# Optimization experiments

Measured on AMD Instinct MI355X. Metric: run time of the kernel, lower is better.

Reference implementation:

```python
import jax, jax.numpy as jnp
import numpy as np

N = 100000
E = 3200000
IN_DIM = 128
HD = 64
HEADS = 4
NEG_SLOPE = 0.2


def setup_inputs() -> dict:
    key = jax.random.key(0)
    ks = jax.random.split(key, 12)
    s = lambda fan_in: 1.0 / np.sqrt(fan_in)
    x = jax.random.normal(ks[0], (N, IN_DIM), dtype=jnp.float32)
    edge_index = jax.random.randint(ks[1], (2, E), 0, N, dtype=jnp.int64)
    W1 = jax.random.normal(ks[2], (IN_DIM, HEADS * HD), dtype=jnp.float32) * s(IN_DIM)
    a_src1 = jax.random.normal(ks[3], (HEADS, HD), dtype=jnp.float32) * s(HD)
    a_dst1 = jax.random.normal(ks[4], (HEADS, HD), dtype=jnp.float32) * s(HD)
    b1 = jnp.zeros((HEADS * HD,), dtype=jnp.float32)
    W2 = jax.random.normal(ks[5], (HEADS * HD, HD), dtype=jnp.float32) * s(HEADS * HD)
    a_src2 = jax.random.normal(ks[6], (1, HD), dtype=jnp.float32) * s(HD)
    a_dst2 = jax.random.normal(ks[7], (1, HD), dtype=jnp.float32) * s(HD)
    b2 = jnp.zeros((HD,), dtype=jnp.float32)
    lin_w = jax.random.normal(ks[8], (HD, 2), dtype=jnp.float32) * s(HD)
    lin_b = jnp.zeros((2,), dtype=jnp.float32)
    return {"x": x, "edge_index": edge_index, "W1": W1, "a_src1": a_src1,
            "a_dst1": a_dst1, "b1": b1, "W2": W2, "a_src2": a_src2,
            "a_dst2": a_dst2, "b2": b2, "lin_w": lin_w, "lin_b": lin_b}


def gat_conv(x, src, dst, W, a_src, a_dst, bias, heads, out_dim, concat):
    n = x.shape[0]
    h = (x @ W).reshape(n, heads, out_dim)                 # [N,H,D]
    alpha_s = jnp.einsum('nhd,hd->nh', h, a_src)           # [N,H]
    alpha_d = jnp.einsum('nhd,hd->nh', h, a_dst)           # [N,H]
    e = alpha_s[src] + alpha_d[dst]                        # [Etot,H]
    e = jnp.where(e > 0, e, NEG_SLOPE * e)                 # leaky relu
    m = jax.ops.segment_max(e, dst, num_segments=n)        # scatter-softmax (stable)
    m = jnp.where(jnp.isfinite(m), m, 0.0)
    e = jnp.exp(e - m[dst])
    denom = jax.ops.segment_sum(e, dst, num_segments=n)
    alpha = e / denom[dst]                                 # [Etot,H]
    out = jax.ops.segment_sum(h[src] * alpha[:, :, None], dst, num_segments=n)  # [N,H,D]
    out = out.reshape(n, heads * out_dim) if concat else out.mean(axis=1)
    return out + bias


def reference(x, edge_index, W1, a_src1, a_dst1, b1, W2, a_src2, a_dst2, b2, lin_w, lin_b):
    n = x.shape[0]
    loops = jnp.arange(n, dtype=edge_index.dtype)
    src = jnp.concatenate([edge_index[0], loops])          # add self-loops (PyG default)
    dst = jnp.concatenate([edge_index[1], loops])
    h = gat_conv(x, src, dst, W1, a_src1, a_dst1, b1, HEADS, HD, True)
    h = jax.nn.elu(h)
    h = gat_conv(h, src, dst, W2, a_src2, a_dst2, b2, 1, HD, True)
    h = jax.nn.elu(h)
    return h @ lin_w + lin_b                               # [N,2]
```

## Files before the change

### kernel.cpp

```cpp
#include <hip/hip_runtime.h>
#include <hip/hip_fp16.h>
#include <math.h>

#define NN 100000
#define EE 3200000
#define ETOT (EE + NN)
#define NEG_SLOPE 0.2f
#define DMAX 96
#define CHUNK 4096
#define NB0 ((ETOT + CHUNK - 1) / CHUNK)
#define RB 391
#define CAP 16384
#define PREPB 391

typedef _Float16 half8 __attribute__((ext_vector_type(8)));
typedef _Float16 half4v __attribute__((ext_vector_type(4)));
typedef float floatx4 __attribute__((ext_vector_type(4)));

__device__ __forceinline__ float wsum64(float v) {
#pragma unroll
  for (int o = 32; o; o >>= 1) v += __shfl_xor(v, o);
  return v;
}
__device__ __forceinline__ float lrelu(float v) { return v > 0.f ? v : NEG_SLOPE * v; }
__device__ __forceinline__ float elu1(float v) { return v > 0.f ? v : expm1f(v); }

__global__ void k_init(int* __restrict__ ccur) {
  ccur[threadIdx.x] = threadIdx.x * CAP;
}

__global__ __launch_bounds__(256) void k_pass1(const int* __restrict__ ei,
                                               int* __restrict__ ccur,
                                               unsigned* __restrict__ ebuf,
                                               const float* __restrict__ W1,
                                               const float* __restrict__ W2,
                                               _Float16* __restrict__ W1t,
                                               _Float16* __restrict__ W2t,
                                               const float* __restrict__ x,
                                               const float* __restrict__ a_src1,
                                               const float* __restrict__ a_dst1,
                                               _Float16* __restrict__ xh,
                                               float* __restrict__ as1,
                                               float* __restrict__ ad1) {
  __shared__ __align__(16) char smem[26624];
  const int b = blockIdx.x;
  const int t = threadIdx.x;
  if (b < NB0) {
    unsigned* vv = (unsigned*)smem;
    unsigned short* cbv = (unsigned short*)(smem + 16384);
    int* h = (int*)(smem + 24576);
    int* cur = (int*)(smem + 25600);
    h[t] = 0;
    __syncthreads();
    int base = b * CHUNK;
    int lim = base + CHUNK; if (lim > ETOT) lim = ETOT;
    int cnt = lim - base;
    for (int i = t; i < cnt; i += 256) {
      int e = base + i;
      int s, d;
      if (e < EE) { s = ei[e]; d = ei[EE + e]; } else { s = e - EE; d = s; }
      unsigned cb = (unsigned)d / (unsigned)RB;
      unsigned dloc = (unsigned)d - cb * (unsigned)RB;
      vv[i] = (dloc << 17) | (unsigned)s;
      cbv[i] = (unsigned short)cb;
      atomicAdd(&h[cb], 1);
    }
    __syncthreads();
    if (h[t]) cur[t] = atomicAdd(&ccur[t], h[t]);
    __syncthreads();
    for (int i = t; i < cnt; i += 256) {
      int cb = cbv[i];
      int pos = atomicAdd(&cur[cb], 1);
      ebuf[pos] = vv[i];
    }
    return;
  }
  if (b < NB0 + 192) {
    int idx = (b - NB0) * 256 + t;
    if (idx < 32768) {
      int n = idx >> 7, k = idx & 127;
      W1t[idx] = (_Float16)W1[k * 256 + n];
    } else {
      int j = idx - 32768;
      int n = j >> 8, k = j & 255;
      W2t[j] = (_Float16)W2[k * 64 + n];
    }
    return;
  }
  float* vs = (float*)smem;
  float* vd = vs + 512;
  for (int i = t; i < 512; i += 256) {
    int h = i >> 7, k = i & 127;
    const float* wrow = W1 + (size_t)k * 256 + h * 64;
    float ss = 0.f, dd = 0.f;
#pragma unroll 8
    for (int d2 = 0; d2 < 64; ++d2) {
      float wv = wrow[d2];
      ss = fmaf(wv, a_src1[h * 64 + d2], ss);
      dd = fmaf(wv, a_dst1[h * 64 + d2], dd);
    }
    vs[i] = ss; vd[i] = dd;
  }
  __syncthreads();
  const int lane = t & 63;
  const int sub8 = lane >> 3;
  const int dl = lane & 7;
  const int gw = (b - NB0 - 192) * 4 + (t >> 6);
  for (int nb = gw * 8; nb < NN; nb += 4 * PREPB * 8) {
    const int n = nb + sub8;
    const bool ok = n < NN;
    float4 xv[4];
#pragma unroll
    for (int j = 0; j < 4; ++j)
      xv[j] = ok ? *(const float4*)(x + (size_t)n * 128 + dl * 16 + j * 4)
                 : make_float4(0.f, 0.f, 0.f, 0.f);
    const float* xf = (const float*)xv;
    if (ok) {
      half8 h0, h1;
#pragma unroll
      for (int c = 0; c < 8; ++c) { h0[c] = (_Float16)xf[c]; h1[c] = (_Float16)xf[8 + c]; }
      *(half8*)(xh + (size_t)n * 128 + dl * 16) = h0;
      *(half8*)(xh + (size_t)n * 128 + dl * 16 + 8) = h1;
    }
    float p[8];
#pragma unroll
    for (int h = 0; h < 4; ++h) {
      float ss = 0.f, dd = 0.f;
#pragma unroll
      for (int c = 0; c < 16; ++c) {
        float xc = xf[c];
        ss = fmaf(xc, vs[h * 128 + dl * 16 + c], ss);
        dd = fmaf(xc, vd[h * 128 + dl * 16 + c], dd);
      }
      p[h] = ss; p[4 + h] = dd;
    }
#pragma unroll
    for (int j = 0; j < 8; ++j) {
      p[j] += __shfl_xor(p[j], 1);
      p[j] += __shfl_xor(p[j], 2);
      p[j] += __shfl_xor(p[j], 4);
    }
    if (ok && dl == 0) {
      *(float4*)(as1 + n * 4) = make_float4(p[0], p[1], p[2], p[3]);
      *(float4*)(ad1 + n * 4) = make_float4(p[4], p[5], p[6], p[7]);
    }
  }
}

__global__ __launch_bounds__(256) void k_pass2(const unsigned* __restrict__ ebuf,
                                               const int* __restrict__ ccur,
                                               int* __restrict__ offs,
                                               int* __restrict__ degarr,
                                               int* __restrict__ csr) {
  __shared__ unsigned ed[CAP];
  __shared__ int hist[RB];
  __shared__ int cur[RB];
  int b = blockIdx.x, t = threadIdx.x;
  int d0 = b * RB;
  int rb = NN - d0; if (rb > RB) rb = RB;
  int w0 = b * CAP;
  int cnt = ccur[b] - w0;
  if (cnt > CAP) cnt = CAP;
  for (int j = t; j < rb; j += 256) hist[j] = 0;
  __syncthreads();
  for (int i = t; i < cnt; i += 256) {
    unsigned v = ebuf[w0 + i];
    ed[i] = v;
    atomicAdd(&hist[v >> 17], 1);
  }
  __syncthreads();
  if (t == 0) {
    int run = w0;
    for (int j = 0; j < rb; ++j) { cur[j] = run; run += hist[j]; }
  }
  __syncthreads();
  for (int j = t; j < rb; j += 256) {
    offs[d0 + j] = cur[j];
    degarr[d0 + j] = hist[j];
  }
  __syncthreads();
  for (int i = t; i < cnt; i += 256) {
    unsigned v = ed[i];
    int pos = atomicAdd(&cur[v >> 17], 1);
    csr[pos] = (int)(v & 0x1FFFFu);
  }
}

__global__ __launch_bounds__(256) void k_agg1(const int* __restrict__ offs,
                                              const int* __restrict__ degarr,
                                              const int* __restrict__ csr_src,
                                              const float* __restrict__ a_s,
                                              const float* __restrict__ a_d,
                                              const _Float16* __restrict__ xh,
                                              _Float16* __restrict__ agg) {
  __shared__ __align__(16) float alp[4][DMAX][4];
  __shared__ int sidx[4][DMAX];
  const int wid = threadIdx.x >> 6;
  const int n = blockIdx.x * 4 + wid;
  const int lane = threadIdx.x & 63;
  const int beg = offs[n], deg = degarr[n];
  const float4 ad = *(const float4*)(a_d + n * 4);
  float4 sm = make_float4(0.f, 0.f, 0.f, 0.f);
  for (int d = lane; d < deg; d += 64) {
    int s = csr_src[beg + d];
    float4 as = *(const float4*)(a_s + s * 4);
    float e0 = __expf(lrelu(as.x + ad.x));
    float e1 = __expf(lrelu(as.y + ad.y));
    float e2 = __expf(lrelu(as.z + ad.z));
    float e3 = __expf(lrelu(as.w + ad.w));
    sm.x += e0; sm.y += e1; sm.z += e2; sm.w += e3;
    if (d < DMAX) {
      sidx[wid][d] = s;
      *(float4*)&alp[wid][d][0] = make_float4(e0, e1, e2, e3);
    }
  }
  sm.x = wsum64(sm.x); sm.y = wsum64(sm.y); sm.z = wsum64(sm.z); sm.w = wsum64(sm.w);
  const float4 inv4 = make_float4(1.f / sm.x, 1.f / sm.y, 1.f / sm.z, 1.f / sm.w);
  const int dlim = deg < DMAX ? deg : DMAX;
  for (int d = lane; d < dlim; d += 64) {
    float4 a = *(float4*)&alp[wid][d][0];
    a.x *= inv4.x; a.y *= inv4.y; a.z *= inv4.z; a.w *= inv4.w;
    *(float4*)&alp[wid][d][0] = a;
  }
  const int g = lane >> 4;
  const int sub = lane & 15;
  const _Float16* __restrict__ hb = xh + sub * 8;
  float acc[4][8];
#pragma unroll
  for (int h = 0; h < 4; ++h)
#pragma unroll
    for (int j = 0; j < 8; ++j) acc[h][j] = 0.f;
  int d = 0;
  for (; d + 8 <= dlim; d += 8) {
    int i0 = d + g, i1 = d + 4 + g;
    int s0 = sidx[wid][i0], s1 = sidx[wid][i1];
    float4 w0 = *(float4*)&alp[wid][i0][0];
    float4 w1 = *(float4*)&alp[wid][i1][0];
    half8 r0 = *(const half8*)(hb + (size_t)s0 * 128);
    half8 r1 = *(const half8*)(hb + (size_t)s1 * 128);
#pragma unroll
    for (int j = 0; j < 8; ++j) {
      float f0 = (float)r0[j], f1 = (float)r1[j];
      acc[0][j] = fmaf(f0, w0.x, acc[0][j]);
      acc[1][j] = fmaf(f0, w0.y, acc[1][j]);
      acc[2][j] = fmaf(f0, w0.z, acc[2][j]);
      acc[3][j] = fmaf(f0, w0.w, acc[3][j]);
      acc[0][j] = fmaf(f1, w1.x, acc[0][j]);
      acc[1][j] = fmaf(f1, w1.y, acc[1][j]);
      acc[2][j] = fmaf(f1, w1.z, acc[2][j]);
      acc[3][j] = fmaf(f1, w1.w, acc[3][j]);
    }
  }
  if (d + 4 <= dlim) {
    int i0 = d + g;
    int s0 = sidx[wid][i0];
    float4 w0 = *(float4*)&alp[wid][i0][0];
    half8 r0 = *(const half8*)(hb + (size_t)s0 * 128);
#pragma unroll
    for (int j = 0; j < 8; ++j) {
      float f0 = (float)r0[j];
      acc[0][j] = fmaf(f0, w0.x, acc[0][j]);
      acc[1][j] = fmaf(f0, w0.y, acc[1][j]);
      acc[2][j] = fmaf(f0, w0.z, acc[2][j]);
      acc[3][j] = fmaf(f0, w0.w, acc[3][j]);
    }
    d += 4;
  }
  if (d < dlim) {
    int idx = d + g;
    bool v = idx < dlim;
    int s = sidx[wid][v ? idx : d];
    float4 w0 = *(float4*)&alp[wid][v ? idx : d][0];
    if (!v) { w0.x = 0.f; w0.y = 0.f; w0.z = 0.f; w0.w = 0.f; }
    half8 r0 = *(const half8*)(hb + (size_t)s * 128);
#pragma unroll
    for (int j = 0; j < 8; ++j) {
      float f0 = (float)r0[j];
      acc[0][j] = fmaf(f0, w0.x, acc[0][j]);
      acc[1][j] = fmaf(f0, w0.y, acc[1][j]);
      acc[2][j] = fmaf(f0, w0.z, acc[2][j]);
      acc[3][j] = fmaf(f0, w0.w, acc[3][j]);
    }
  }
  if (deg > DMAX) {
    for (int dd = DMAX + g; dd < deg; dd += 4) {
      int s = csr_src[beg + dd];
      float4 as = *(const float4*)(a_s + s * 4);
      float w0x = __expf(lrelu(as.x + ad.x)) * inv4.x;
      float w0y = __expf(lrelu(as.y + ad.y)) * inv4.y;
      float w0z = __expf(lrelu(as.z + ad.z)) * inv4.z;
      float w0w = __expf(lrelu(as.w + ad.w)) * inv4.w;
      half8 r0 = *(const half8*)(hb + (size_t)s * 128);
#pragma unroll
      for (int j = 0; j < 8; ++j) {
        float f0 = (float)r0[j];
        acc[0][j] = fmaf(f0, w0x, acc[0][j]);
        acc[1][j] = fmaf(f0, w0y, acc[1][j]);
        acc[2][j] = fmaf(f0, w0z, acc[2][j]);
        acc[3][j] = fmaf(f0, w0w, acc[3][j]);
      }
    }
  }
#pragma unroll
  for (int h = 0; h < 4; ++h)
#pragma unroll
    for (int j = 0; j < 8; ++j) {
      acc[h][j] += __shfl_xor(acc[h][j], 16);
      acc[h][j] += __shfl_xor(acc[h][j], 32);
    }
  if (g == 0) {
#pragma unroll
    for (int h = 0; h < 4; ++h) {
      half8 o;
#pragma unroll
      for (int j = 0; j < 8; ++j) o[j] = (_Float16)acc[h][j];
      *(half8*)(agg + ((size_t)n * 4 + h) * 128 + sub * 8) = o;
    }
  }
}

__global__ __launch_bounds__(256) void k_gemmAgg2(const _Float16* __restrict__ agg,
                                                  const _Float16* __restrict__ W1t,
                                                  const _Float16* __restrict__ W2t,
                                                  const float* __restrict__ b1,
                                                  const float* __restrict__ a_src2,
                                                  const float* __restrict__ a_dst2,
                                                  _Float16* __restrict__ h2h,
                                                  float* __restrict__ as_out,
                                                  float* __restrict__ ad_out) {
  __shared__ __align__(16) _Float16 As[32][520];
  __shared__ __align__(16) _Float16 h1eT[32][264];
  __shared__ float prt[2][4][32];
  const int tid = threadIdx.x;
  const int row0 = blockIdx.x * 32;
#pragma unroll
  for (int i = 0; i < 8; ++i) {
    int c = i * 256 + tid;
    int r = c >> 6;
    int c8 = c & 63;
    *(half8*)&As[r][c8 * 8] = *(const half8*)(agg + (size_t)(row0 + r) * 512 + c8 * 8);
  }
  __syncthreads();
  const int wid = tid >> 6, lane = tid & 63;
  const int m16 = lane & 15, quad = lane >> 4;
  floatx4 acc1[2][4];
#pragma unroll
  for (int mt = 0; mt < 2; ++mt)
#pragma unroll
    for (int nt = 0; nt < 4; ++nt) acc1[mt][nt] = (floatx4){0.f, 0.f, 0.f, 0.f};
#pragma unroll
  for (int mt = 0; mt < 2; ++mt) {
#pragma unroll
    for (int ks = 0; ks < 4; ++ks) {
      half8 av = *(half8*)&As[mt * 16 + m16][wid * 128 + ks * 32 + quad * 8];
#pragma unroll
      for (int nt = 0; nt < 4; ++nt) {
        half8 bv = *(const half8*)(W1t + (size_t)(wid * 64 + nt * 16 + m16) * 128 + ks * 32 + quad * 8);
        acc1[mt][nt] = __builtin_amdgcn_mfma_f32_16x16x32_f16(av, bv, acc1[mt][nt], 0, 0, 0);
      }
    }
  }
#pragma unroll
  for (int mt = 0; mt < 2; ++mt)
#pragma unroll
    for (int nt = 0; nt < 4; ++nt) {
      float bb = b1[wid * 64 + nt * 16 + m16];
#pragma unroll
      for (int r = 0; r < 4; ++r)
        h1eT[mt * 16 + quad * 4 + r][wid * 64 + nt * 16 + m16] = (_Float16)elu1(acc1[mt][nt][r] + bb);
    }
  __syncthreads();
  floatx4 acc2[2];
#pragma unroll
  for (int mt = 0; mt < 2; ++mt) acc2[mt] = (floatx4){0.f, 0.f, 0.f, 0.f};
#pragma unroll
  for (int mt = 0; mt < 2; ++mt) {
#pragma unroll
    for (int ks = 0; ks < 8; ++ks) {
      half8 av = *(half8*)&h1eT[mt * 16 + m16][ks * 32 + quad * 8];
      half8 bv = *(const half8*)(W2t + (size_t)(wid * 16 + m16) * 256 + ks * 32 + quad * 8);
      acc2[mt] = __builtin_amdgcn_mfma_f32_16x16x32_f16(av, bv, acc2[mt], 0, 0, 0);
    }
  }
  const float a2v = a_src2[wid * 16 + m16];
  const float d2v = a_dst2[wid * 16 + m16];
#pragma unroll
  for (int mt = 0; mt < 2; ++mt)
#pragma unroll
    for (int r = 0; r < 4; ++r) {
      int row = mt * 16 + quad * 4 + r;
      h2h[(size_t)(row0 + row) * 64 + wid * 16 + m16] = (_Float16)acc2[mt][r];
      float ps = acc2[mt][r] * a2v, pd = acc2[mt][r] * d2v;
#pragma unroll
      for (int o = 1; o < 16; o <<= 1) { ps += __shfl_xor(ps, o); pd += __shfl_xor(pd, o); }
      if (m16 == 0) { prt[0][wid][row] = ps; prt[1][wid][row] = pd; }
    }
  __syncthreads();
  if (tid < 32) {
    as_out[row0 + tid] = prt[0][0][tid] + prt[0][1][tid] + prt[0][2][tid] + prt[0][3][tid];
    ad_out[row0 + tid] = prt[1][0][tid] + prt[1][1][tid] + prt[1][2][tid] + prt[1][3][tid];
  }
}

__global__ __launch_bounds__(256) void k_attn2(const int* __restrict__ offs,
                                               const int* __restrict__ degarr,
                                               const int* __restrict__ csr_src,
                                               const float* __restrict__ a_s,
                                               const float* __restrict__ a_d,
                                               const _Float16* __restrict__ h2h,
                                               const float* __restrict__ b2,
                                               const float* __restrict__ lin_w,
                                               const float* __restrict__ lin_b,
                                               float* __restrict__ out) {
  __shared__ float alpha2[4][DMAX];
  __shared__ int sidx2[4][DMAX];
  const int wid = threadIdx.x >> 6;
  const int n = blockIdx.x * 4 + wid;
  const int lane = threadIdx.x & 63;
  const int beg = offs[n], deg = degarr[n];
  const float adn = a_d[n];
  float sm = 0.f;
  for (int d = lane; d < deg; d += 64) {
    int s = csr_src[beg + d];
    float e = __expf(lrelu(a_s[s] + adn));
    sm += e;
    if (d < DMAX) { sidx2[wid][d] = s; alpha2[wid][d] = e; }
  }
  sm = wsum64(sm);
  const float inv = 1.f / sm;
  const int dlim = deg < DMAX ? deg : DMAX;
  for (int d = lane; d < dlim; d += 64) alpha2[wid][d] *= inv;
  const int g = lane >> 4;
  const int sub = lane & 15;
  const _Float16* __restrict__ hb = h2h + sub * 4;
  float a0 = 0.f, a1 = 0.f, a2 = 0.f, a3 = 0.f;
  int d = 0;
  for (; d + 8 <= dlim; d += 8) {
    int i0 = d + g, i1 = d + 4 + g;
    int s0 = sidx2[wid][i0], s1 = sidx2[wid][i1];
    float w0 = alpha2[wid][i0], w1 = alpha2[wid][i1];
    half4v r0 = *(const half4v*)(hb + (size_t)s0 * 64);
    half4v r1 = *(const half4v*)(hb + (size_t)s1 * 64);
    a0 = fmaf((float)r0[0], w0, a0); a1 = fmaf((float)r0[1], w0, a1);
    a2 = fmaf((float)r0[2], w0, a2); a3 = fmaf((float)r0[3], w0, a3);
    a0 = fmaf((float)r1[0], w1, a0); a1 = fmaf((float)r1[1], w1, a1);
    a2 = fmaf((float)r1[2], w1, a2); a3 = fmaf((float)r1[3], w1, a3);
  }
  if (d + 4 <= dlim) {
    int i0 = d + g;
    int s0 = sidx2[wid][i0];
    float w0 = alpha2[wid][i0];
    half4v r0 = *(const half4v*)(hb + (size_t)s0 * 64);
    a0 = fmaf((float)r0[0], w0, a0); a1 = fmaf((float)r0[1], w0, a1);
    a2 = fmaf((float)r0[2], w0, a2); a3 = fmaf((float)r0[3], w0, a3);
    d += 4;
  }
  if (d < dlim) {
    int idx = d + g;
    bool v = idx < dlim;
    int s = sidx2[wid][v ? idx : d];
    float w = v ? alpha2[wid][idx] : 0.f;
    half4v r = *(const half4v*)(hb + (size_t)s * 64);
    a0 = fmaf((float)r[0], w, a0); a1 = fmaf((float)r[1], w, a1);
    a2 = fmaf((float)r[2], w, a2); a3 = fmaf((float)r[3], w, a3);
  }
  if (deg > DMAX && g == 0) {
    for (int dd = DMAX; dd < deg; ++dd) {
      int s = csr_src[beg + dd];
      float w = __expf(lrelu(a_s[s] + adn)) * inv;
      half4v r = *(const half4v*)(hb + (size_t)s * 64);
      a0 = fmaf((float)r[0], w, a0); a1 = fmaf((float)r[1], w, a1);
      a2 = fmaf((float)r[2], w, a2); a3 = fmaf((float)r[3], w, a3);
    }
  }
  a0 += __shfl_xor(a0, 16); a1 += __shfl_xor(a1, 16);
  a2 += __shfl_xor(a2, 16); a3 += __shfl_xor(a3, 16);
  a0 += __shfl_xor(a0, 32); a1 += __shfl_xor(a1, 32);
  a2 += __shfl_xor(a2, 32); a3 += __shfl_xor(a3, 32);
  const int c = sub * 4;
  float4 bb = *(const float4*)(b2 + c);
  float o0 = elu1(a0 + bb.x);
  float o1 = elu1(a1 + bb.y);
  float o2 = elu1(a2 + bb.z);
  float o3 = elu1(a3 + bb.w);
  float4 lw0 = *(const float4*)(lin_w + c * 2);
  float4 lw1 = *(const float4*)(lin_w + c * 2 + 4);
  float p0 = o0 * lw0.x + o1 * lw0.z + o2 * lw1.x + o3 * lw1.z;
  float p1 = o0 * lw0.y + o1 * lw0.w + o2 * lw1.y + o3 * lw1.w;
  p0 = wsum64(p0) * 0.25f;
  p1 = wsum64(p1) * 0.25f;
  if (lane == 0) {
    out[n * 2 + 0] = p0 + lin_b[0];
    out[n * 2 + 1] = p1 + lin_b[1];
  }
}

extern "C" void kernel_launch(void* const* d_in, const int* in_sizes, int n_in,
                              void* d_out, int out_size, void* d_ws, size_t ws_size,
                              hipStream_t stream) {
  const float* x      = (const float*)d_in[0];
  const int*   ei     = (const int*)d_in[1];
  const float* W1     = (const float*)d_in[2];
  const float* a_src1 = (const float*)d_in[3];
  const float* a_dst1 = (const float*)d_in[4];
  const float* b1     = (const float*)d_in[5];
  const float* W2     = (const float*)d_in[6];
  const float* a_src2 = (const float*)d_in[7];
  const float* a_dst2 = (const float*)d_in[8];
  const float* b2     = (const float*)d_in[9];
  const float* lin_w  = (const float*)d_in[10];
  const float* lin_b  = (const float*)d_in[11];
  float* outp = (float*)d_out;

  char* w = (char*)d_ws;
  _Float16* agg  = (_Float16*)(w + 0);
  unsigned* ebuf = (unsigned*)(w + 33554432);
  _Float16* xh   = (_Float16*)(w + 102400000);
  _Float16* h2h  = (_Float16*)(w + 102400000);
  int*    csr    = (int*)(w + 128000000);
  _Float16* W1t  = (_Float16*)(w + 144777216);
  _Float16* W2t  = (_Float16*)(w + 144842752);
  float*  as1    = (float*)(w + 144875520);
  float*  ad1    = (float*)(w + 146475520);
  float*  as2    = (float*)(w + 148075520);
  float*  ad2    = (float*)(w + 148475520);
  int*    offs   = (int*)(w + 148875520);
  int*    degarr = (int*)(w + 149275520);
  int*    ccur   = (int*)(w + 149675520);

  k_init<<<1, 256, 0, stream>>>(ccur);
  k_pass1<<<NB0 + 192 + PREPB, 256, 0, stream>>>(ei, ccur, ebuf, W1, W2, W1t, W2t,
                                                 x, a_src1, a_dst1, xh, as1, ad1);
  k_pass2<<<256, 256, 0, stream>>>(ebuf, ccur, offs, degarr, csr);

  k_agg1<<<NN / 4, 256, 0, stream>>>(offs, degarr, csr, as1, ad1, xh, agg);
  k_gemmAgg2<<<NN / 32, 256, 0, stream>>>(agg, W1t, W2t, b1, a_src2, a_dst2, h2h, as2, ad2);

  k_attn2<<<NN / 4, 256, 0, stream>>>(offs, degarr, csr, as2, ad2, h2h, b2, lin_w, lin_b, outp);
}
```

Measured before the change: 507.7 us.

## Restructure graph preprocessing kernels and unroll gather loops by four

New measurement: 557.4 us. 9.8% more time.

```diff
diff --git a/kernel.cpp b/kernel.cpp
--- a/kernel.cpp
+++ b/kernel.cpp
@@ -11,7 +11,8 @@
 #define NB0 ((ETOT + CHUNK - 1) / CHUNK)
 #define RB 391
 #define CAP 16384
-#define PREPB 391
+#define WPB 48
+#define XPB 104
 
 typedef _Float16 half8 __attribute__((ext_vector_type(8)));
 typedef _Float16 half4v __attribute__((ext_vector_type(4)));
@@ -29,54 +30,100 @@
   ccur[threadIdx.x] = threadIdx.x * CAP;
 }
 
-__global__ __launch_bounds__(256) void k_pass1(const int* __restrict__ ei,
-                                               int* __restrict__ ccur,
-                                               unsigned* __restrict__ ebuf,
-                                               const float* __restrict__ W1,
-                                               const float* __restrict__ W2,
-                                               _Float16* __restrict__ W1t,
-                                               _Float16* __restrict__ W2t,
-                                               const float* __restrict__ x,
-                                               const float* __restrict__ a_src1,
-                                               const float* __restrict__ a_dst1,
-                                               _Float16* __restrict__ xh,
-                                               float* __restrict__ as1,
-                                               float* __restrict__ ad1) {
-  __shared__ __align__(16) char smem[26624];
+__global__ __launch_bounds__(256) void k_bucket(const int* __restrict__ ei,
+                                                int* __restrict__ ccur,
+                                                unsigned* __restrict__ ebuf) {
+  __shared__ unsigned vv[CHUNK];
+  __shared__ unsigned short cbv[CHUNK];
+  __shared__ int h[256];
+  __shared__ int cur[256];
   const int b = blockIdx.x;
   const int t = threadIdx.x;
-  if (b < NB0) {
-    unsigned* vv = (unsigned*)smem;
-    unsigned short* cbv = (unsigned short*)(smem + 16384);
-    int* h = (int*)(smem + 24576);
-    int* cur = (int*)(smem + 25600);
-    h[t] = 0;
+  h[t] = 0;
+  __syncthreads();
+  int base = b * CHUNK;
+  int lim = base + CHUNK; if (lim > ETOT) lim = ETOT;
+  int cnt = lim - base;
+  for (int i = t; i < cnt; i += 256) {
+    int e = base + i;
+    int s, d;
+    if (e < EE) { s = ei[e]; d = ei[EE + e]; } else { s = e - EE; d = s; }
+    unsigned cb = (unsigned)d / (unsigned)RB;
+    unsigned dloc = (unsigned)d - cb * (unsigned)RB;
+    vv[i] = (dloc << 17) | (unsigned)s;
+    cbv[i] = (unsigned short)cb;
+    atomicAdd(&h[cb], 1);
+  }
+  __syncthreads();
+  if (h[t]) cur[t] = atomicAdd(&ccur[t], h[t]);
+  __syncthreads();
+  for (int i = t; i < cnt; i += 256) {
+    int cb = cbv[i];
+    int pos = atomicAdd(&cur[cb], 1);
+    ebuf[pos] = vv[i];
+  }
+}
+
+__global__ __launch_bounds__(1024) void k_build(const unsigned* __restrict__ ebuf,
+                                                const int* __restrict__ ccur,
+                                                int* __restrict__ offs,
+                                                int* __restrict__ degarr,
+                                                int* __restrict__ csr,
+                                                const float* __restrict__ W1,
+                                                const float* __restrict__ W2,
+                                                _Float16* __restrict__ W1t,
+                                                _Float16* __restrict__ W2t,
+                                                const float* __restrict__ x,
+                                                const float* __restrict__ a_src1,
+                                                const float* __restrict__ a_dst1,
+                                                _Float16* __restrict__ xh,
+                                                float* __restrict__ as1,
+                                                float* __restrict__ ad1) {
+  __shared__ int hist[RB];
+  __shared__ int cur[RB];
+  __shared__ int sc[2][512];
+  const int b = blockIdx.x;
+  const int t = threadIdx.x;
+  if (b < 256) {
+    const int d0 = b * RB;
+    int rb = NN - d0; if (rb > RB) rb = RB;
+    const int w0 = b * CAP;
+    int cnt = ccur[b] - w0;
+    if (cnt > CAP) cnt = CAP;
+    for (int j = t; j < rb; j += 1024) hist[j] = 0;
     __syncthreads();
-    int base = b * CHUNK;
-    int lim = base + CHUNK; if (lim > ETOT) lim = ETOT;
-    int cnt = lim - base;
-    for (int i = t; i < cnt; i += 256) {
-      int e = base + i;
-      int s, d;
-      if (e < EE) { s = ei[e]; d = ei[EE + e]; } else { s = e - EE; d = s; }
-      unsigned cb = (unsigned)d / (unsigned)RB;
-      unsigned dloc = (unsigned)d - cb * (unsigned)RB;
-      vv[i] = (dloc << 17) | (unsigned)s;
-      cbv[i] = (unsigned short)cb;
-      atomicAdd(&h[cb], 1);
-    }
+    for (int i = t; i < cnt; i += 1024)
+      atomicAdd(&hist[ebuf[w0 + i] >> 17], 1);
     __syncthreads();
-    if (h[t]) cur[t] = atomicAdd(&ccur[t], h[t]);
+    if (t < 512) sc[0][t] = (t < rb) ? hist[t] : 0;
     __syncthreads();
-    for (int i = t; i < cnt; i += 256) {
-      int cb = cbv[i];
-      int pos = atomicAdd(&cur[cb], 1);
-      ebuf[pos] = vv[i];
+    int sb = 0;
+#pragma unroll
+    for (int off = 1; off < 512; off <<= 1) {
+      if (t < 512) {
+        int v = sc[sb][t];
+        if (t >= off) v += sc[sb][t - off];
+        sc[sb ^ 1][t] = v;
+      }
+      __syncthreads();
+      sb ^= 1;
+    }
+    for (int j = t; j < rb; j += 1024) {
+      int ex = j ? sc[sb][j - 1] : 0;
+      offs[d0 + j] = w0 + ex;
+      degarr[d0 + j] = hist[j];
+      cur[j] = w0 + ex;
+    }
+    __syncthreads();
+    for (int i = t; i < cnt; i += 1024) {
+      unsigned v = ebuf[w0 + i];
+      int pos = atomicAdd(&cur[v >> 17], 1);
+      csr[pos] = (int)(v & 0x1FFFFu);
     }
     return;
   }
-  if (b < NB0 + 192) {
-    int idx = (b - NB0) * 256 + t;
+  if (b < 256 + WPB) {
+    int idx = (b - 256) * 1024 + t;
     if (idx < 32768) {
       int n = idx >> 7, k = idx & 127;
       W1t[idx] = (_Float16)W1[k * 256 + n];
@@ -87,9 +134,9 @@
     }
     return;
   }
-  float* vs = (float*)smem;
+  float* vs = (float*)sc;
   float* vd = vs + 512;
-  for (int i = t; i < 512; i += 256) {
+  for (int i = t; i < 512; i += 1024) {
     int h = i >> 7, k = i & 127;
     const float* wrow = W1 + (size_t)k * 256 + h * 64;
     float ss = 0.f, dd = 0.f;
@@ -105,8 +152,8 @@
   const int lane = t & 63;
   const int sub8 = lane >> 3;
   const int dl = lane & 7;
-  const int gw = (b - NB0 - 192) * 4 + (t >> 6);
-  for (int nb = gw * 8; nb < NN; nb += 4 * PREPB * 8) {
+  const int gw = (b - 256 - WPB) * 16 + (t >> 6);
+  for (int nb = gw * 8; nb < NN; nb += 16 * XPB * 8) {
     const int n = nb + sub8;
     const bool ok = n < NN;
     float4 xv[4];
@@ -144,45 +191,6 @@
       *(float4*)(as1 + n * 4) = make_float4(p[0], p[1], p[2], p[3]);
       *(float4*)(ad1 + n * 4) = make_float4(p[4], p[5], p[6], p[7]);
     }
-  }
-}
-
-__global__ __launch_bounds__(256) void k_pass2(const unsigned* __restrict__ ebuf,
-                                               const int* __restrict__ ccur,
-                                               int* __restrict__ offs,
-                                               int* __restrict__ degarr,
-                                               int* __restrict__ csr) {
-  __shared__ unsigned ed[CAP];
-  __shared__ int hist[RB];
-  __shared__ int cur[RB];
-  int b = blockIdx.x, t = threadIdx.x;
-  int d0 = b * RB;
-  int rb = NN - d0; if (rb > RB) rb = RB;
-  int w0 = b * CAP;
-  int cnt = ccur[b] - w0;
-  if (cnt > CAP) cnt = CAP;
-  for (int j = t; j < rb; j += 256) hist[j] = 0;
-  __syncthreads();
-  for (int i = t; i < cnt; i += 256) {
-    unsigned v = ebuf[w0 + i];
-    ed[i] = v;
-    atomicAdd(&hist[v >> 17], 1);
-  }
-  __syncthreads();
-  if (t == 0) {
-    int run = w0;
-    for (int j = 0; j < rb; ++j) { cur[j] = run; run += hist[j]; }
-  }
-  __syncthreads();
-  for (int j = t; j < rb; j += 256) {
-    offs[d0 + j] = cur[j];
-    degarr[d0 + j] = hist[j];
-  }
-  __syncthreads();
-  for (int i = t; i < cnt; i += 256) {
-    unsigned v = ed[i];
-    int pos = atomicAdd(&cur[v >> 17], 1);
-    csr[pos] = (int)(v & 0x1FFFFu);
   }
 }
 
@@ -231,6 +239,30 @@
 #pragma unroll
     for (int j = 0; j < 8; ++j) acc[h][j] = 0.f;
   int d = 0;
+  for (; d + 16 <= dlim; d += 16) {
+    int ss[4]; float4 wv[4];
+#pragma unroll
+    for (int u = 0; u < 4; ++u) {
+      int idx = d + u * 4 + g;
+      ss[u] = sidx[wid][idx];
+      wv[u] = *(float4*)&alp[wid][idx][0];
+    }
+    half8 rr[4];
+#pragma unroll
+    for (int u = 0; u < 4; ++u)
+      rr[u] = *(const half8*)(hb + (size_t)ss[u] * 128);
+#pragma unroll
+    for (int u = 0; u < 4; ++u) {
+#pragma unroll
+      for (int j = 0; j < 8; ++j) {
+        float f = (float)rr[u][j];
+        acc[0][j] = fmaf(f, wv[u].x, acc[0][j]);
+        acc[1][j] = fmaf(f, wv[u].y, acc[1][j]);
+        acc[2][j] = fmaf(f, wv[u].z, acc[2][j]);
+        acc[3][j] = fmaf(f, wv[u].w, acc[3][j]);
+      }
+    }
+  }
   for (; d + 8 <= dlim; d += 8) {
     int i0 = d + g, i1 = d + 4 + g;
     int s0 = sidx[wid][i0], s1 = sidx[wid][i1];
@@ -435,6 +467,24 @@
   const _Float16* __restrict__ hb = h2h + sub * 4;
   float a0 = 0.f, a1 = 0.f, a2 = 0.f, a3 = 0.f;
   int d = 0;
+  for (; d + 16 <= dlim; d += 16) {
+    int ss[4]; float ww[4];
+#pragma unroll
+    for (int u = 0; u < 4; ++u) {
+      int idx = d + u * 4 + g;
+      ss[u] = sidx2[wid][idx];
+      ww[u] = alpha2[wid][idx];
+    }
+    half4v rr[4];
+#pragma unroll
+    for (int u = 0; u < 4; ++u)
+      rr[u] = *(const half4v*)(hb + (size_t)ss[u] * 64);
+#pragma unroll
+    for (int u = 0; u < 4; ++u) {
+      a0 = fmaf((float)rr[u][0], ww[u], a0); a1 = fmaf((float)rr[u][1], ww[u], a1);
+      a2 = fmaf((float)rr[u][2], ww[u], a2); a3 = fmaf((float)rr[u][3], ww[u], a3);
+    }
+  }
   for (; d + 8 <= dlim; d += 8) {
     int i0 = d + g, i1 = d + 4 + g;
     int s0 = sidx2[wid][i0], s1 = sidx2[wid][i1];
@@ -529,9 +579,10 @@
   int*    ccur   = (int*)(w + 149675520);
 
   k_init<<<1, 256, 0, stream>>>(ccur);
-  k_pass1<<<NB0 + 192 + PREPB, 256, 0, stream>>>(ei, ccur, ebuf, W1, W2, W1t, W2t,
-                                                 x, a_src1, a_dst1, xh, as1, ad1);
-  k_pass2<<<256, 256, 0, stream>>>(ebuf, ccur, offs, degarr, csr);
+  k_bucket<<<NB0, 256, 0, stream>>>(ei, ccur, ebuf);
+  k_build<<<256 + WPB + XPB, 1024, 0, stream>>>(ebuf, ccur, offs, degarr, csr,
+                                                W1, W2, W1t, W2t,
+                                                x, a_src1, a_dst1, xh, as1, ad1);
 
   k_agg1<<<NN / 4, 256, 0, stream>>>(offs, degarr, csr, as1, ad1, xh, agg);
   k_gemmAgg2<<<NN / 32, 256, 0, stream>>>(agg, W1t, W2t, b1, a_src2, a_dst2, h2h, as2, ad2);
```

## Sub-bucket edges by source octant so CSR neighbor lists are source-sorted

Applied to the files above, without the earlier changes.

Result: slower. 525.4 us (+3.5%).

```diff
diff --git a/kernel.cpp b/kernel.cpp
--- a/kernel.cpp
+++ b/kernel.cpp
@@ -10,7 +10,9 @@
 #define CHUNK 4096
 #define NB0 ((ETOT + CHUNK - 1) / CHUNK)
 #define RB 391
-#define CAP 16384
+#define NOCT 8
+#define CAP_O 2560
+#define WCAP 16384
 #define PREPB 391
 
 typedef _Float16 half8 __attribute__((ext_vector_type(8)));
@@ -26,7 +28,8 @@
 __device__ __forceinline__ float elu1(float v) { return v > 0.f ? v : expm1f(v); }
 
 __global__ void k_init(int* __restrict__ ccur) {
-  ccur[threadIdx.x] = threadIdx.x * CAP;
+  int i = blockIdx.x * 256 + threadIdx.x;
+  ccur[i] = i * CAP_O;
 }
 
 __global__ __launch_bounds__(256) void k_pass1(const int* __restrict__ ei,
@@ -42,15 +45,15 @@
                                                _Float16* __restrict__ xh,
                                                float* __restrict__ as1,
                                                float* __restrict__ ad1) {
-  __shared__ __align__(16) char smem[26624];
+  __shared__ __align__(16) char smem[40960];
   const int b = blockIdx.x;
   const int t = threadIdx.x;
   if (b < NB0) {
     unsigned* vv = (unsigned*)smem;
     unsigned short* cbv = (unsigned short*)(smem + 16384);
     int* h = (int*)(smem + 24576);
-    int* cur = (int*)(smem + 25600);
-    h[t] = 0;
+    int* cur = (int*)(smem + 32768);
+    for (int i = t; i < 2048; i += 256) h[i] = 0;
     __syncthreads();
     int base = b * CHUNK;
     int lim = base + CHUNK; if (lim > ETOT) lim = ETOT;
@@ -61,16 +64,19 @@
       if (e < EE) { s = ei[e]; d = ei[EE + e]; } else { s = e - EE; d = s; }
       unsigned cb = (unsigned)d / (unsigned)RB;
       unsigned dloc = (unsigned)d - cb * (unsigned)RB;
+      unsigned oct = (unsigned)s / 12500u;
+      unsigned key = cb * NOCT + oct;
       vv[i] = (dloc << 17) | (unsigned)s;
-      cbv[i] = (unsigned short)cb;
-      atomicAdd(&h[cb], 1);
+      cbv[i] = (unsigned short)key;
+      atomicAdd(&h[key], 1);
     }
     __syncthreads();
-    if (h[t]) cur[t] = atomicAdd(&ccur[t], h[t]);
+    for (int k = t; k < 2048; k += 256)
+      if (h[k]) cur[k] = atomicAdd(&ccur[k], h[k]);
     __syncthreads();
     for (int i = t; i < cnt; i += 256) {
-      int cb = cbv[i];
-      int pos = atomicAdd(&cur[cb], 1);
+      int key = cbv[i];
+      int pos = atomicAdd(&cur[key], 1);
       ebuf[pos] = vv[i];
     }
     return;
@@ -152,25 +158,43 @@
                                                int* __restrict__ offs,
                                                int* __restrict__ degarr,
                                                int* __restrict__ csr) {
-  __shared__ unsigned ed[CAP];
+  __shared__ unsigned ed[WCAP];
   __shared__ int hist[RB];
   __shared__ int cur[RB];
+  __shared__ int ocnt[NOCT];
+  __shared__ int obase[NOCT + 1];
   int b = blockIdx.x, t = threadIdx.x;
   int d0 = b * RB;
   int rb = NN - d0; if (rb > RB) rb = RB;
-  int w0 = b * CAP;
-  int cnt = ccur[b] - w0;
-  if (cnt > CAP) cnt = CAP;
+  if (t < NOCT) {
+    int k = b * NOCT + t;
+    int c = ccur[k] - k * CAP_O;
+    if (c > CAP_O) c = CAP_O;
+    ocnt[t] = c;
+  }
   for (int j = t; j < rb; j += 256) hist[j] = 0;
   __syncthreads();
-  for (int i = t; i < cnt; i += 256) {
-    unsigned v = ebuf[w0 + i];
-    ed[i] = v;
-    atomicAdd(&hist[v >> 17], 1);
-  }
-  __syncthreads();
   if (t == 0) {
-    int run = w0;
+    obase[0] = 0;
+    for (int o = 0; o < NOCT; ++o) {
+      int c = ocnt[o];
+      if (obase[o] + c > WCAP) c = WCAP - obase[o];
+      obase[o + 1] = obase[o] + c;
+    }
+  }
+  __syncthreads();
+  for (int o = 0; o < NOCT; ++o) {
+    int base = obase[o], cnt_o = obase[o + 1] - base;
+    int w0 = (b * NOCT + o) * CAP_O;
+    for (int i = t; i < cnt_o; i += 256) {
+      unsigned v = ebuf[w0 + i];
+      ed[base + i] = v;
+      atomicAdd(&hist[v >> 17], 1);
+    }
+  }
+  __syncthreads();
+  if (t == 0) {
+    int run = b * WCAP;
     for (int j = 0; j < rb; ++j) { cur[j] = run; run += hist[j]; }
   }
   __syncthreads();
@@ -179,10 +203,14 @@
     degarr[d0 + j] = hist[j];
   }
   __syncthreads();
-  for (int i = t; i < cnt; i += 256) {
-    unsigned v = ed[i];
-    int pos = atomicAdd(&cur[v >> 17], 1);
-    csr[pos] = (int)(v & 0x1FFFFu);
+  for (int o = 0; o < NOCT; ++o) {
+    int base = obase[o], cnt_o = obase[o + 1] - base;
+    for (int i = t; i < cnt_o; i += 256) {
+      unsigned v = ed[base + i];
+      int pos = atomicAdd(&cur[v >> 17], 1);
+      csr[pos] = (int)(v & 0x1FFFFu);
+    }
+    __syncthreads();
   }
 }
 
@@ -528,7 +556,7 @@
   int*    degarr = (int*)(w + 149275520);
   int*    ccur   = (int*)(w + 149675520);
 
-  k_init<<<1, 256, 0, stream>>>(ccur);
+  k_init<<<8, 256, 0, stream>>>(ccur);
   k_pass1<<<NB0 + 192 + PREPB, 256, 0, stream>>>(ei, ccur, ebuf, W1, W2, W1t, W2t,
                                                  x, a_src1, a_dst1, xh, as1, ad1);
   k_pass2<<<256, 256, 0, stream>>>(ebuf, ccur, offs, degarr, csr);
```
